# Kernel tuning notes

Hardware: AMD Instinct MI355X
Metric: run time of the kernel (lower is better)

Reference implementation:

```python
import jax, jax.numpy as jnp
import numpy as np

D = 256
H = 8
DH = D // H
N = 100000
B = 256
T = 131072
HID_FUSE = 256   # fuse MLP hidden = d_model
HID_HEAD = 256   # QuantileHeads hidden
NQ = 3           # quantiles (q10, q50, q90)


def setup_inputs() -> dict:
    key = jax.random.key(0)
    ks = jax.random.split(key, 32)
    p = lambda k, *s: (0.02 * jax.random.normal(k, s, dtype=jnp.float32))
    inp = {
        'node_embeddings': jax.random.normal(ks[0], (N, D), dtype=jnp.float32),
        'target_index': jax.random.randint(ks[1], (B,), 0, N),
        'port_index': jax.random.randint(ks[2], (T,), 0, N),
        'port_batch': jnp.sort(jax.random.randint(ks[3], (T,), 0, B)),
        'port_weight': jax.random.uniform(ks[4], (T,), dtype=jnp.float32),
        # PMA pooling params (learnable seed + MHA projections, no biases)
        'seed': p(ks[5], D),
        'Wq_p': p(ks[6], D, D), 'Wk_p': p(ks[7], D, D), 'Wv_p': p(ks[8], D, D), 'Wo_p': p(ks[9], D, D),
        # target->portfolio cross-attention params
        'Wq_c': p(ks[10], D, D), 'Wk_c': p(ks[11], D, D), 'Wv_c': p(ks[12], D, D), 'Wo_c': p(ks[13], D, D),
        # fuse LayerNorm(3d) + MLP
        'ln_g': jnp.ones((3 * D,), jnp.float32), 'ln_b': jnp.zeros((3 * D,), jnp.float32),
        'fuse_W1': p(ks[14], 3 * D, HID_FUSE), 'fuse_b1': jnp.zeros((HID_FUSE,), jnp.float32),
        'fuse_W2': p(ks[15], HID_FUSE, D), 'fuse_b2': jnp.zeros((D,), jnp.float32),
        # quantile heads MLP
        'head_W1': p(ks[16], D, HID_HEAD), 'head_b1': jnp.zeros((HID_HEAD,), jnp.float32),
        'head_W2': p(ks[17], HID_HEAD, NQ), 'head_b2': jnp.zeros((NQ,), jnp.float32),
    }
    return inp


def _segment_attend(logits, v, seg, num_segments):
    # logits [T,H], v [T,H,DH], seg [T] -> pooled [num_segments, H, DH]
    m = jax.ops.segment_max(logits, seg, num_segments=num_segments)  # [B,H]
    e = jnp.exp(logits - m[seg])                                      # [T,H]
    s = jax.ops.segment_sum(e, seg, num_segments=num_segments)        # [B,H]
    p = e / (s[seg] + 1e-9)
    return jax.ops.segment_sum(p[..., None] * v, seg, num_segments=num_segments)


def reference(node_embeddings, target_index, port_index, port_batch, port_weight,
              seed, Wq_p, Wk_p, Wv_p, Wo_p, Wq_c, Wk_c, Wv_c, Wo_c,
              ln_g, ln_b, fuse_W1, fuse_b1, fuse_W2, fuse_b2,
              head_W1, head_b1, head_W2, head_b2):
    b = target_index.shape[0]
    scale = float(DH) ** -0.5
    tgt = node_embeddings[target_index]          # [B,D]
    tok = node_embeddings[port_index]            # [T,D]
    logw = jnp.log(port_weight + 1e-8)           # DV01 weighting as logit bias

    # --- PMA: learnable seed query pools DV01-weighted portfolio tokens ---
    q_p = (seed @ Wq_p).reshape(H, DH)
    k_p = (tok @ Wk_p).reshape(-1, H, DH)
    v_p = (tok @ Wv_p).reshape(-1, H, DH)
    lg_p = jnp.einsum('thd,hd->th', k_p, q_p) * scale + logw[:, None]
    pooled = _segment_attend(lg_p, v_p, port_batch, b).reshape(b, D)
    contexts = pooled @ Wo_p                     # [B,D]; zeros for empty portfolios

    # --- target -> portfolio cross-attention (residual) ---
    q_c = (tgt @ Wq_c).reshape(b, H, DH)
    k_c = (tok @ Wk_c).reshape(-1, H, DH)
    v_c = (tok @ Wv_c).reshape(-1, H, DH)
    lg_c = jnp.einsum('thd,thd->th', k_c, q_c[port_batch]) * scale + logw[:, None]
    att = _segment_attend(lg_c, v_c, port_batch, b).reshape(b, D)
    fused = tgt + att @ Wo_c                     # [B,D]; == tgt for empty portfolios

    # --- fuse: concat -> LN -> MLP ---
    z = jnp.concatenate([tgt, contexts, fused], axis=-1)  # [B,3D]
    mu = jnp.mean(z, axis=-1, keepdims=True)
    var = jnp.var(z, axis=-1, keepdims=True)
    z = (z - mu) * jax.lax.rsqrt(var + 1e-5) * ln_g + ln_b
    z = jax.nn.relu(z @ fuse_W1 + fuse_b1) @ fuse_W2 + fuse_b2  # [B,D]

    # --- quantile heads ---
    out = jax.nn.relu(z @ head_W1 + head_b1) @ head_W2 + head_b2  # [B,NQ]
    return out
```

## Files before the change

### kernel.cpp

```cpp
#include <hip/hip_runtime.h>
#include <hip/hip_bf16.h>

typedef __attribute__((ext_vector_type(8))) short short8;
typedef __attribute__((ext_vector_type(4))) float floatx4;

#define SCALE 0.17677669529663687f

__device__ __forceinline__ unsigned short f2bf(float f) {
  unsigned int x = __float_as_uint(f);
  x += 0x7fffu + ((x >> 16) & 1u);
  return (unsigned short)(x >> 16);
}
__device__ __forceinline__ float bf2f(unsigned short u) {
  return __uint_as_float(((unsigned int)u) << 16);
}

__device__ __forceinline__ short8 load_cvt8(const float* p) {
  floatx4 a = *(const floatx4*)p;
  floatx4 b = *(const floatx4*)(p + 4);
  short8 r;
  r[0] = (short)f2bf(a[0]); r[1] = (short)f2bf(a[1]);
  r[2] = (short)f2bf(a[2]); r[3] = (short)f2bf(a[3]);
  r[4] = (short)f2bf(b[0]); r[5] = (short)f2bf(b[1]);
  r[6] = (short)f2bf(b[2]); r[7] = (short)f2bf(b[3]);
  return r;
}

__global__ __launch_bounds__(256) void k_qc_gemm(
    const float* __restrict__ node, const int* __restrict__ tgt_idx,
    const float* __restrict__ seed,
    const float* __restrict__ Wq_c, const float* __restrict__ Wq_p,
    float* __restrict__ q_all, int B)
{
  __shared__ float act_l[4 * 256];
  const int tid = threadIdx.x;
  const int bt = blockIdx.x, nt = blockIdx.y;
  const int BT = B >> 2;
  for (int i = tid; i < 4 * 256; i += 256) {
    int m = i >> 8, k = i & 255;
    int b = bt * 4 + m;
    float v = 0.f;
    if (b < B)       v = node[(size_t)tgt_idx[b] * 256 + k];
    else if (b == B) v = seed[k];
    act_l[i] = v;
  }
  __syncthreads();
  const float* W = (bt == BT) ? Wq_p : Wq_c;
  const int m = tid >> 6, lane = tid & 63, ks = lane >> 4, n = lane & 15;
  const int n0 = nt * 16;
  float acc = 0.f;
  const float* Wp = W + (size_t)(ks * 64) * 256 + n0 + n;
  const float* ap = &act_l[m * 256 + ks * 64];
  #pragma unroll 8
  for (int k = 0; k < 64; ++k) acc += ap[k] * Wp[(size_t)k * 256];
  acc += __shfl_xor(acc, 16, 64);
  acc += __shfl_xor(acc, 32, 64);
  const int b = bt * 4 + m;
  if (ks == 0 && b <= B) q_all[(size_t)b * 256 + n0 + n] = acc;
}

__global__ __launch_bounds__(256) void k_fold(
    const float* __restrict__ Wk_c, const float* __restrict__ Wk_p,
    const float* __restrict__ q_all, const int* __restrict__ port_batch,
    unsigned short* __restrict__ u_c_all, unsigned short* __restrict__ u_p_t,
    int* __restrict__ seg, int T, int B)
{
  const int tid = threadIdx.x;
  const int bt = blockIdx.x, dt = blockIdx.y;
  const int BT = B >> 2;
  if (dt == 0) {
    int key = -1;
    if (bt < BT) { if (tid < 4) key = bt * 4 + tid; }
    else if (tid == 0) key = B;
    if (key >= 0) {
      int lo = 0, hi = T;
      while (lo < hi) { int mid = (lo + hi) >> 1; if (port_batch[mid] < key) lo = mid + 1; else hi = mid; }
      seg[key] = lo;
    }
  }
  const int m = tid >> 6, lane = tid & 63;
  const int b = bt * 4 + m;
  if (b > B) return;
  const float* Wk = (b == B) ? Wk_p : Wk_c;
  const float* q = q_all + (size_t)b * 256;
  #pragma unroll
  for (int t2 = 0; t2 < 2; ++t2) {
    const int idx = t2 * 64 + lane;
    const int h = idx >> 4;
    const int d = dt * 16 + (idx & 15);
    float acc = 0.f;
    const float* wr = Wk + (size_t)d * 256 + h * 32;
    const float* qr = q + h * 32;
    #pragma unroll 8
    for (int j = 0; j < 32; ++j) acc += wr[j] * qr[j];
    unsigned short v = f2bf(acc);
    if (b < B) u_c_all[(size_t)b * 2048 + h * 256 + d] = v;
    else       u_p_t[h * 256 + d] = v;
  }
}

__global__ __launch_bounds__(256, 2) void attn_kernel(
    const float* __restrict__ node,
    const int* __restrict__ port_index,
    const float* __restrict__ port_weight,
    const unsigned short* __restrict__ u_p_t,
    const unsigned short* __restrict__ u_c_all,
    const int* __restrict__ seg,
    float* __restrict__ slabs, int T, int S)
{
  __shared__ __align__(16) unsigned short tok_lds[64 * 264];
  __shared__ __align__(16) unsigned short E_t[16 * 72];
  __shared__ float l_lds[16];

  const int tid  = threadIdx.x;
  const int s    = blockIdx.x;
  const int b    = blockIdx.y;
  const int lane = tid & 63;
  const int w    = tid >> 6;
  const int q    = lane >> 4;
  const int n    = lane & 15;

  if (tid < 16) l_lds[tid] = 0.f;

  short8 ufrag[8];
  const unsigned short* ubase = (n < 8) ? (u_p_t + n * 256)
                                        : (u_c_all + (size_t)b * 2048 + (n - 8) * 256);
  #pragma unroll
  for (int s8 = 0; s8 < 8; ++s8)
    ufrag[s8] = *(const short8*)(ubase + q * 8 + s8 * 32);

  const int start  = seg[b];
  const int end    = seg[b + 1];
  const int ntiles = (end - start + 63) >> 6;

  floatx4 sacc[4];
  #pragma unroll
  for (int nt = 0; nt < 4; ++nt) sacc[nt] = (floatx4){0.f, 0.f, 0.f, 0.f};

  __syncthreads();

  for (int it = s; it < ntiles; it += S) {
    const int tbase = start + it * 64;
    short8 cur[8];
    {
      int t = tbase + w * 16 + n; int tc = t < T ? t : T - 1;
      const float* rp = node + (size_t)port_index[tc] * 256 + q * 8;
      #pragma unroll
      for (int k = 0; k < 8; ++k) cur[k] = load_cvt8(rp + k * 32);
    }
    float pw[4];
    #pragma unroll
    for (int r = 0; r < 4; ++r) { int tr = tbase + w * 16 + q * 4 + r; pw[r] = port_weight[tr < T ? tr : T - 1]; }

    floatx4 lacc = (floatx4){0.f, 0.f, 0.f, 0.f};
    #pragma unroll
    for (int k = 0; k < 8; ++k)
      lacc = __builtin_amdgcn_mfma_f32_16x16x32_bf16(cur[k], ufrag[k], lacc, 0, 0, 0);
    float lsum = 0.f;
    #pragma unroll
    for (int r = 0; r < 4; ++r) {
      const int tr = tbase + w * 16 + q * 4 + r;
      float e = 0.f;
      if (tr < end) {
        float lg = lacc[r] * SCALE + logf(pw[r] + 1e-8f);
        e = __expf(lg);
      }
      unsigned short eb = f2bf(e);
      E_t[n * 72 + w * 16 + q * 4 + r] = eb;
      lsum += bf2f(eb);
    }
    lsum += __shfl_xor(lsum, 16, 64);
    lsum += __shfl_xor(lsum, 32, 64);
    if (lane < 16) atomicAdd(&l_lds[lane], lsum);
    #pragma unroll
    for (int k = 0; k < 8; ++k)
      *(short8*)(tok_lds + (w * 16 + n) * 264 + q * 8 + k * 32) = cur[k];
    __syncthreads();
    short8 ea0 = *(const short8*)(E_t + n * 72 + q * 8);
    short8 ea1 = *(const short8*)(E_t + n * 72 + 32 + q * 8);
    #pragma unroll
    for (int nt = 0; nt < 4; ++nt) {
      const int dcol = w * 64 + nt * 16 + n;
      short8 b0, b1;
      #pragma unroll
      for (int j = 0; j < 8; ++j) b0[j] = (short)tok_lds[(q * 8 + j) * 264 + dcol];
      #pragma unroll
      for (int j = 0; j < 8; ++j) b1[j] = (short)tok_lds[(32 + q * 8 + j) * 264 + dcol];
      sacc[nt] = __builtin_amdgcn_mfma_f32_16x16x32_bf16(ea0, b0, sacc[nt], 0, 0, 0);
      sacc[nt] = __builtin_amdgcn_mfma_f32_16x16x32_bf16(ea1, b1, sacc[nt], 0, 0, 0);
    }
    __syncthreads();
  }

  float* stage = (float*)tok_lds;
  #pragma unroll
  for (int nt = 0; nt < 4; ++nt)
    #pragma unroll
    for (int r = 0; r < 4; ++r)
      stage[(q * 4 + r) * 256 + w * 64 + nt * 16 + n] = sacc[nt][r];
  __syncthreads();
  float* sl = slabs + ((size_t)b * S + s) * 4224;
  #pragma unroll
  for (int i = 0; i < 4; ++i) {
    const int row = i * 4 + w;
    const int c0 = (tid & 63) * 4;
    *(floatx4*)(sl + row * 256 + c0) = *(const floatx4*)(stage + row * 256 + c0);
  }
  if (tid < 16) sl[4096 + tid] = l_lds[tid];
}

__global__ __launch_bounds__(256) void k_slab_gemm(
    const float* __restrict__ slabs, int S,
    const float* __restrict__ Wv_p, const float* __restrict__ Wv_c,
    float* __restrict__ X)
{
  __shared__ float act_l[4 * 256];
  __shared__ float lsum[4];
  const int tid = threadIdx.x;
  const int bt = blockIdx.x, nt = blockIdx.y, z = blockIdx.z;
  const int head = nt >> 1;
  const int row = z * 8 + head;
  if (tid < 4) {
    const float* sl = slabs + (size_t)(bt * 4 + tid) * S * 4224;
    float l = 0.f;
    for (int s = 0; s < S; ++s) l += sl[s * 4224 + 4096 + row];
    lsum[tid] = 1.0f / (l + 1e-9f);
  }
  __syncthreads();
  for (int i = tid; i < 4 * 256; i += 256) {
    int m = i >> 8, k = i & 255;
    const float* sl = slabs + (size_t)(bt * 4 + m) * S * 4224;
    float sum = 0.f;
    for (int s = 0; s < S; ++s) sum += sl[s * 4224 + row * 256 + k];
    act_l[i] = sum * lsum[m];
  }
  __syncthreads();
  const int m = tid >> 6, lane = tid & 63, ks = lane >> 4, n = lane & 15;
  const int n0 = nt * 16;
  const float* W = z ? Wv_c : Wv_p;
  float acc = 0.f;
  const float* Wp = W + (size_t)(ks * 64) * 256 + n0 + n;
  const float* ap = &act_l[m * 256 + ks * 64];
  #pragma unroll 8
  for (int k = 0; k < 64; ++k) acc += ap[k] * Wp[(size_t)k * 256];
  acc += __shfl_xor(acc, 16, 64);
  acc += __shfl_xor(acc, 32, 64);
  if (ks == 0)
    X[(size_t)(bt * 4 + m) * 512 + z * 256 + n0 + n] = acc;
}

__global__ __launch_bounds__(256) void k_plain_gemm(
    const float* __restrict__ act, int act_ld,
    const float* __restrict__ W0, const float* __restrict__ W1,
    const float* __restrict__ bias0, const float* __restrict__ bias1,
    float* __restrict__ outp, int out_ld,
    int K, int relu)
{
  __shared__ float act_l[4 * 768];
  const int tid = threadIdx.x;
  const int bt = blockIdx.x, nt = blockIdx.y, z = blockIdx.z;
  const float* W = z ? W1 : W0;
  const float* bias = z ? bias1 : bias0;
  for (int i = tid; i < 4 * K; i += 256) {
    int m = i / K, k = i - m * K;
    act_l[m * K + k] = act[(size_t)(bt * 4 + m) * act_ld + z * K + k];
  }
  __syncthreads();
  const int m = tid >> 6, lane = tid & 63, ks = lane >> 4, n = lane & 15;
  const int n0 = nt * 16;
  const int Kq = K >> 2;
  float acc = 0.f;
  const float* Wp = W + (size_t)(ks * Kq) * 256 + n0 + n;
  const float* ap = &act_l[m * K + ks * Kq];
  #pragma unroll 8
  for (int k = 0; k < Kq; ++k) acc += ap[k] * Wp[(size_t)k * 256];
  acc += __shfl_xor(acc, 16, 64);
  acc += __shfl_xor(acc, 32, 64);
  if (ks == 0) {
    float v = acc + (bias ? bias[n0 + n] : 0.f);
    if (relu) v = fmaxf(v, 0.f);
    outp[(size_t)(bt * 4 + m) * out_ld + z * 256 + n0 + n] = v;
  }
}

__global__ __launch_bounds__(256) void k_ln_gemm(
    const float* __restrict__ node, const int* __restrict__ tgt_idx,
    const float* __restrict__ zbuf,
    const float* __restrict__ ln_g, const float* __restrict__ ln_b,
    const float* __restrict__ fuse_W1, const float* __restrict__ fuse_b1,
    float* __restrict__ h1)
{
  __shared__ float act_l[4 * 768];
  const int tid = threadIdx.x;
  const int bt = blockIdx.x, nt = blockIdx.y;
  for (int i = tid; i < 4 * 256; i += 256) {
    int m = i >> 8, k = i & 255;
    int b = bt * 4 + m;
    float tg = node[(size_t)tgt_idx[b] * 256 + k];
    float C  = zbuf[(size_t)b * 512 + k];
    float Fp = zbuf[(size_t)b * 512 + 256 + k];
    act_l[m * 768 + k]       = tg;
    act_l[m * 768 + 256 + k] = C;
    act_l[m * 768 + 512 + k] = tg + Fp;
  }
  __syncthreads();
  const int m = tid >> 6, lane = tid & 63;
  {
    float s = 0.f;
    for (int k = lane; k < 768; k += 64) s += act_l[m * 768 + k];
    #pragma unroll
    for (int o = 32; o >= 1; o >>= 1) s += __shfl_xor(s, o, 64);
    const float mu = s * (1.0f / 768.0f);
    float v = 0.f;
    for (int k = lane; k < 768; k += 64) { float d = act_l[m * 768 + k] - mu; v += d * d; }
    #pragma unroll
    for (int o = 32; o >= 1; o >>= 1) v += __shfl_xor(v, o, 64);
    const float rstd = 1.0f / sqrtf(v * (1.0f / 768.0f) + 1e-5f);
    for (int k = lane; k < 768; k += 64)
      act_l[m * 768 + k] = (act_l[m * 768 + k] - mu) * rstd * ln_g[k] + ln_b[k];
  }
  __syncthreads();
  const int ks = lane >> 4, n = lane & 15;
  const int n0 = nt * 16;
  float acc = 0.f;
  const float* Wp = fuse_W1 + (size_t)(ks * 192) * 256 + n0 + n;
  const float* ap = &act_l[m * 768 + ks * 192];
  #pragma unroll 8
  for (int k = 0; k < 192; ++k) acc += ap[k] * Wp[(size_t)k * 256];
  acc += __shfl_xor(acc, 16, 64);
  acc += __shfl_xor(acc, 32, 64);
  if (ks == 0)
    h1[(size_t)(bt * 4 + m) * 256 + n0 + n] = fmaxf(acc + fuse_b1[n0 + n], 0.f);
}

__global__ __launch_bounds__(256) void k_outhead(
    const float* __restrict__ hh, const float* __restrict__ head_W2,
    const float* __restrict__ head_b2, float* __restrict__ out)
{
  const int tid = threadIdx.x;
  const int m = tid >> 6, lane = tid & 63;
  const int b = blockIdx.x * 4 + m;
  float a0 = 0.f, a1 = 0.f, a2 = 0.f;
  for (int k = lane; k < 256; k += 64) {
    float h = hh[(size_t)b * 256 + k];
    a0 += h * head_W2[k * 3 + 0];
    a1 += h * head_W2[k * 3 + 1];
    a2 += h * head_W2[k * 3 + 2];
  }
  #pragma unroll
  for (int o = 32; o >= 1; o >>= 1) {
    a0 += __shfl_xor(a0, o, 64);
    a1 += __shfl_xor(a1, o, 64);
    a2 += __shfl_xor(a2, o, 64);
  }
  if (lane == 0) {
    out[b * 3 + 0] = a0 + head_b2[0];
    out[b * 3 + 1] = a1 + head_b2[1];
    out[b * 3 + 2] = a2 + head_b2[2];
  }
}

extern "C" void kernel_launch(void* const* d_in, const int* in_sizes, int n_in,
                              void* d_out, int out_size, void* d_ws, size_t ws_size,
                              hipStream_t stream) {
  const float* node        = (const float*)d_in[0];
  const int*   tgt_idx     = (const int*)d_in[1];
  const int*   port_index  = (const int*)d_in[2];
  const int*   port_batch  = (const int*)d_in[3];
  const float* port_weight = (const float*)d_in[4];
  const float* seed        = (const float*)d_in[5];
  const float* Wq_p = (const float*)d_in[6];
  const float* Wk_p = (const float*)d_in[7];
  const float* Wv_p = (const float*)d_in[8];
  const float* Wo_p = (const float*)d_in[9];
  const float* Wq_c = (const float*)d_in[10];
  const float* Wk_c = (const float*)d_in[11];
  const float* Wv_c = (const float*)d_in[12];
  const float* Wo_c = (const float*)d_in[13];
  const float* ln_g = (const float*)d_in[14];
  const float* ln_b = (const float*)d_in[15];
  const float* fuse_W1 = (const float*)d_in[16];
  const float* fuse_b1 = (const float*)d_in[17];
  const float* fuse_W2 = (const float*)d_in[18];
  const float* fuse_b2 = (const float*)d_in[19];
  const float* head_W1 = (const float*)d_in[20];
  const float* head_b1 = (const float*)d_in[21];
  const float* head_W2 = (const float*)d_in[22];
  const float* head_b2 = (const float*)d_in[23];

  const int B = in_sizes[1];
  const int T = in_sizes[2];

  char* ws = (char*)d_ws;
  unsigned short* u_p_t   = (unsigned short*)ws;
  int*            seg     = (int*)(ws + 4096);
  unsigned short* u_c_all = (unsigned short*)(ws + 8192);
  float* X    = (float*)(ws + 8192);
  float* zbuf = (float*)(ws + 8192 + (size_t)B * 2048);
  size_t slab_off = 8192 + (size_t)B * 4096;
  float* slabs = (float*)(ws + slab_off);
  float* h1 = slabs;
  float* z2 = h1 + (size_t)B * 256;
  float* hh = z2 + (size_t)B * 256;

  size_t per_slice = (size_t)B * 4224 * 4;
  size_t q_off = slab_off + 8 * per_slice;
  float* q_all = (float*)(ws + q_off);

  int S = 1;
  if (ws_size > slab_off + per_slice) {
    size_t fit = (ws_size - slab_off - ((size_t)(B + 1) * 1024 + 4096)) / per_slice;
    S = (int)(fit < 1 ? 1 : (fit > 8 ? 8 : fit));
  }
  if (S < 8) q_all = (float*)(ws + slab_off + (size_t)S * per_slice);

  const int BT = B / 4;

  k_qc_gemm<<<dim3(BT + 1, 16), 256, 0, stream>>>(node, tgt_idx, seed,
      Wq_c, Wq_p, q_all, B);
  k_fold<<<dim3(BT + 1, 16), 256, 0, stream>>>(Wk_c, Wk_p, q_all, port_batch,
      u_c_all, u_p_t, seg, T, B);
  attn_kernel<<<dim3(S, B), 256, 0, stream>>>(node, port_index, port_weight,
      u_p_t, u_c_all, seg, slabs, T, S);
  k_slab_gemm<<<dim3(BT, 16, 2), 256, 0, stream>>>(slabs, S, Wv_p, Wv_c, X);
  k_plain_gemm<<<dim3(BT, 16, 2), 256, 0, stream>>>(X, 512, Wo_p, Wo_c,
      nullptr, nullptr, zbuf, 512, 256, 0);
  k_ln_gemm<<<dim3(BT, 16), 256, 0, stream>>>(node, tgt_idx, zbuf,
      ln_g, ln_b, fuse_W1, fuse_b1, h1);
  k_plain_gemm<<<dim3(BT, 16, 1), 256, 0, stream>>>(h1, 256, fuse_W2, nullptr,
      fuse_b2, nullptr, z2, 256, 256, 0);
  k_plain_gemm<<<dim3(BT, 16, 1), 256, 0, stream>>>(z2, 256, head_W1, nullptr,
      head_b1, nullptr, hh, 256, 256, 1);
  k_outhead<<<BT, 256, 0, stream>>>(hh, head_W2, head_b2, (float*)d_out);
}
```

Measured before the change: 320.7 us.

## Coalesce token row gathers via LDS staging and cap attention splits at four

```diff
diff --git a/kernel.cpp b/kernel.cpp
--- a/kernel.cpp
+++ b/kernel.cpp
@@ -13,17 +13,6 @@
 }
 __device__ __forceinline__ float bf2f(unsigned short u) {
   return __uint_as_float(((unsigned int)u) << 16);
-}
-
-__device__ __forceinline__ short8 load_cvt8(const float* p) {
-  floatx4 a = *(const floatx4*)p;
-  floatx4 b = *(const floatx4*)(p + 4);
-  short8 r;
-  r[0] = (short)f2bf(a[0]); r[1] = (short)f2bf(a[1]);
-  r[2] = (short)f2bf(a[2]); r[3] = (short)f2bf(a[3]);
-  r[4] = (short)f2bf(b[0]); r[5] = (short)f2bf(b[1]);
-  r[6] = (short)f2bf(b[2]); r[7] = (short)f2bf(b[3]);
-  return r;
 }
 
 __global__ __launch_bounds__(256) void k_qc_gemm(
@@ -141,12 +130,18 @@
 
   for (int it = s; it < ntiles; it += S) {
     const int tbase = start + it * 64;
-    short8 cur[8];
     {
-      int t = tbase + w * 16 + n; int tc = t < T ? t : T - 1;
-      const float* rp = node + (size_t)port_index[tc] * 256 + q * 8;
+      int t0 = tbase + w * 16 + n;
+      int idxv = port_index[t0 < T ? t0 : T - 1];
       #pragma unroll
-      for (int k = 0; k < 8; ++k) cur[k] = load_cvt8(rp + k * 32);
+      for (int i = 0; i < 16; ++i) {
+        int rb = __shfl(idxv, i, 64);
+        floatx4 v = *(const floatx4*)(node + (size_t)rb * 256 + lane * 4);
+        unsigned int p0 = (unsigned int)f2bf(v[0]) | ((unsigned int)f2bf(v[1]) << 16);
+        unsigned int p1 = (unsigned int)f2bf(v[2]) | ((unsigned int)f2bf(v[3]) << 16);
+        uint2 pk; pk.x = p0; pk.y = p1;
+        *(uint2*)(tok_lds + (w * 16 + i) * 264 + lane * 4) = pk;
+      }
     }
     float pw[4];
     #pragma unroll
@@ -154,8 +149,10 @@
 
     floatx4 lacc = (floatx4){0.f, 0.f, 0.f, 0.f};
     #pragma unroll
-    for (int k = 0; k < 8; ++k)
-      lacc = __builtin_amdgcn_mfma_f32_16x16x32_bf16(cur[k], ufrag[k], lacc, 0, 0, 0);
+    for (int k = 0; k < 8; ++k) {
+      short8 af = *(const short8*)(tok_lds + (w * 16 + n) * 264 + q * 8 + k * 32);
+      lacc = __builtin_amdgcn_mfma_f32_16x16x32_bf16(af, ufrag[k], lacc, 0, 0, 0);
+    }
     float lsum = 0.f;
     #pragma unroll
     for (int r = 0; r < 4; ++r) {
@@ -172,9 +169,6 @@
     lsum += __shfl_xor(lsum, 16, 64);
     lsum += __shfl_xor(lsum, 32, 64);
     if (lane < 16) atomicAdd(&l_lds[lane], lsum);
-    #pragma unroll
-    for (int k = 0; k < 8; ++k)
-      *(short8*)(tok_lds + (w * 16 + n) * 264 + q * 8 + k * 32) = cur[k];
     __syncthreads();
     short8 ea0 = *(const short8*)(E_t + n * 72 + q * 8);
     short8 ea1 = *(const short8*)(E_t + n * 72 + 32 + q * 8);
@@ -404,15 +398,12 @@
   float* hh = z2 + (size_t)B * 256;
 
   size_t per_slice = (size_t)B * 4224 * 4;
-  size_t q_off = slab_off + 8 * per_slice;
-  float* q_all = (float*)(ws + q_off);
-
   int S = 1;
   if (ws_size > slab_off + per_slice) {
     size_t fit = (ws_size - slab_off - ((size_t)(B + 1) * 1024 + 4096)) / per_slice;
-    S = (int)(fit < 1 ? 1 : (fit > 8 ? 8 : fit));
-  }
-  if (S < 8) q_all = (float*)(ws + slab_off + (size_t)S * per_slice);
+    S = (int)(fit < 1 ? 1 : (fit > 4 ? 4 : fit));
+  }
+  float* q_all = (float*)(ws + slab_off + (size_t)S * per_slice);
 
   const int BT = B / 4;
 
```

Result: faster. 303.2 us (-5.4%).
